# Optimization experiments

Measured on AMD Instinct MI355X. Metric: run time of the kernel, lower is better.

Reference implementation:

```python
import jax, jax.numpy as jnp
import numpy as np

B, OBS, LAT, NXT, E, HG, H = 8192, 128, 32, 128, 8, 256, 256


def setup_inputs() -> dict:
    key = jax.random.key(0)
    ks = jax.random.split(key, 20)
    d_in = OBS + LAT

    def w(k, shape, fan_in):
        return jax.random.uniform(k, shape, jnp.float32, -1.0, 1.0) * (np.sqrt(3.0) / np.sqrt(fan_in)).astype(np.float32)

    inp = {
        "x": jax.random.normal(ks[0], (B, OBS), jnp.float32),
        "z": jax.random.normal(ks[1], (B, LAT), jnp.float32),
        # gating MLP: (obs+lat) -> hg -> hg -> hg -> E
        "gw0": w(ks[2], (d_in, HG), d_in), "gb0": jnp.zeros((HG,), jnp.float32),
        "gw1": w(ks[3], (HG, HG), HG),    "gb1": jnp.zeros((HG,), jnp.float32),
        "gw2": w(ks[4], (HG, HG), HG),    "gb2": jnp.zeros((HG,), jnp.float32),
        "gw3": w(ks[5], (HG, E), HG),     "gb3": jnp.zeros((E,), jnp.float32),
        # expert weight stacks (kaiming-uniform-style init, bias = 0.01)
        "w0": w(ks[6], (E, d_in, H), d_in * H),      "b0": jnp.full((E, H), 0.01, jnp.float32),
        "w1": w(ks[7], (E, H + LAT, H), (H + LAT) * H), "b1": jnp.full((E, H), 0.01, jnp.float32),
        "w2": w(ks[8], (E, H + LAT, NXT), (H + LAT) * NXT), "b2": jnp.full((E, NXT), 0.01, jnp.float32),
    }
    return inp


def reference(x, z, gw0, gb0, gw1, gb1, gw2, gb2, gw3, gb3, w0, b0, w1, b1, w2, b2):
    xz = jnp.concatenate((x, z), axis=1)  # [B, obs+lat]
    # gating MLP (ELU activations, linear head) -> softmax coefficients over experts
    g = jax.nn.elu(xz @ gw0 + gb0)
    g = jax.nn.elu(g @ gw1 + gb1)
    g = jax.nn.elu(g @ gw2 + gb2)
    coef = jax.nn.softmax(g @ gw3 + gb3, axis=1)  # [B, E]

    layer_out = x
    for w, b, act in ((w0, b0, jax.nn.elu), (w1, b1, jax.nn.elu), (w2, b2, None)):
        inp = jnp.concatenate((layer_out, z), axis=1)  # [B, i]
        # coefficient-weighted expert mixing fused with the per-sample matvec:
        # equals (coef @ flat_weight).view(B,i,o) consumed by baddbmm in the original
        out = jnp.einsum('bi,eio,be->bo', inp, w, coef) + coef @ b
        layer_out = act(out) if act is not None else out
    return layer_out
```

## Files before the change

kernel.cpp:

```cpp
#include <hip/hip_runtime.h>
#include <hip/hip_bf16.h>

typedef _Float16 half_t;
typedef __attribute__((ext_vector_type(8))) _Float16 half8;
typedef __attribute__((ext_vector_type(4))) _Float16 half4;
typedef __attribute__((ext_vector_type(4))) float float4v;

#define BSZ 8192
#define NT 1024
#define ACTSTR 280
#define XSTR 152
#define ZSTR 40

#define RING_SLOT 1024
#define RING_WAVE (3 * RING_SLOT)
#define OFF_SX   (16 * RING_WAVE)
#define OFF_SB0  (OFF_SX + 32 * XSTR)
#define OFF_SB1  (OFF_SB0 + 32 * ACTSTR)
#define OFF_SZ   (OFF_SB1 + 32 * ACTSTR)
#define HALFS_TOTAL (OFF_SZ + 32 * ZSTR)
#define OFF_BIAS_B (HALFS_TOTAL * 2)
#define OFF_LOG_B  (OFF_BIAS_B + 8192)
#define OFF_CF_B   (OFF_LOG_B + 1024)
#define SMEM_BYTES (OFF_CF_B + 1024)

__device__ __forceinline__ float elu_fast(float v) {
    return v > 0.f ? v : (__expf(v) - 1.f);
}

template <int N>
__device__ __forceinline__ void wait_vm() {
    if constexpr (N == 0)      asm volatile("s_waitcnt vmcnt(0)" ::: "memory");
    else if constexpr (N == 1) asm volatile("s_waitcnt vmcnt(1)" ::: "memory");
    else if constexpr (N == 2) asm volatile("s_waitcnt vmcnt(2)" ::: "memory");
    else                       asm volatile("s_waitcnt vmcnt(4)" ::: "memory");
}

__device__ __forceinline__ void lds_dma16(half_t* lds, const half_t* g) {
    __builtin_amdgcn_global_load_lds(
        (const __attribute__((address_space(1))) void*)g,
        (__attribute__((address_space(3))) void*)lds, 16, 0, 0);
}

template <int EXPP, int NPASS, int CH, int MT, bool ZLAST, int ACT, int DST>
__device__ __forceinline__ void layer_run(
    half_t* sm, const half_t* sSrc, int sstr,
    const half_t* __restrict__ W, int NS,
    const float* __restrict__ bias, int biasN, const float* sCf, float* sBias,
    half_t* sDst, float* __restrict__ gOut, int ldg,
    int row0, int strip, int mrow, int wv, int lane, int l15, int quad) {
    constexpr int TOT = NPASS * CH;
    const size_t estr = (size_t)NS * CH * 512;
    const int col = strip * 16 + l15;
    half_t* ring = sm + wv * RING_WAVE;
    const half_t* sZ = sm + OFF_SZ;
    float* myBias = sBias + wv * 128;

    if (quad == 0) {
#pragma unroll
        for (int e = 0; e < NPASS * EXPP; ++e)
            myBias[e * 16 + l15] = bias[e * biasN + col];
    }
    wait_vm<0>();

    float4v acc[EXPP][MT];
    float part[MT][4];

    const half_t* wp = W + (size_t)strip * CH * 512 + lane * 8;
    int s_i = 0, c_i = 0;
    auto issue = [&]() {
        half_t* slot = ring + s_i * RING_SLOT;
#pragma unroll
        for (int e = 0; e < EXPP; ++e) lds_dma16(slot + e * 512, wp + (size_t)e * estr);
        s_i = (s_i == 2) ? 0 : s_i + 1;
        wp += 512;
        if (++c_i == CH) { c_i = 0; wp += EXPP * estr - CH * 512; }
    };

    const half_t* aBase = sSrc + (mrow + l15) * sstr + quad * 8;
    const half_t* zBase = sZ + (mrow + l15) * ZSTR + quad * 8;
    int s_c = 0, c_c = 0, h_c = 0;
    auto body = [&]() {
        half8 a[MT];
#pragma unroll
        for (int mt = 0; mt < MT; ++mt)
            a[mt] = (ZLAST && c_c == CH - 1)
                        ? *(const half8*)&zBase[mt * 16 * ZSTR]
                        : *(const half8*)&aBase[mt * 16 * sstr + c_c * 32];
        if (c_c == 0) {
#pragma unroll
            for (int e = 0; e < EXPP; ++e)
#pragma unroll
                for (int mt = 0; mt < MT; ++mt) acc[e][mt] = (float4v){0.f, 0.f, 0.f, 0.f};
        }
        const half_t* slot = ring + s_c * RING_SLOT + lane * 8;
#pragma unroll
        for (int e = 0; e < EXPP; ++e) {
            half8 b = *(const half8*)&slot[e * 512];
#pragma unroll
            for (int mt = 0; mt < MT; ++mt)
                acc[e][mt] = __builtin_amdgcn_mfma_f32_16x16x32_f16(a[mt], b, acc[e][mt], 0, 0, 0);
        }
        if (c_c == CH - 1) {
            const int eoff = h_c * EXPP;
#pragma unroll
            for (int mt = 0; mt < MT; ++mt)
#pragma unroll
                for (int r = 0; r < 4; ++r) {
                    const int rl = mrow + mt * 16 + quad * 4 + r;
                    float val = 0.f;
#pragma unroll
                    for (int e = 0; e < EXPP; ++e) {
                        const float ab = acc[e][mt][r] + myBias[(eoff + e) * 16 + l15];
                        val += (EXPP * NPASS == 1) ? ab : sCf[rl * 8 + eoff + e] * ab;
                    }
                    part[mt][r] = (h_c == 0) ? val : part[mt][r] + val;
                    if (h_c == NPASS - 1) {
                        float o = part[mt][r];
                        if (DST == 0) {
                            if (ACT) o = elu_fast(o);
                            sDst[rl * ACTSTR + col] = (half_t)o;
                        } else {
                            gOut[(size_t)(row0 + rl) * ldg + col] = o;
                        }
                    }
                }
        }
        s_c = (s_c == 2) ? 0 : s_c + 1;
        if (++c_c == CH) { c_c = 0; ++h_c; }
    };

    issue();
    issue();
#pragma unroll 1
    for (int it = 0; it < TOT - 2; ++it) {
        issue();
        wait_vm<2 * EXPP>();
        body();
    }
    wait_vm<EXPP>();
    body();
    wait_vm<0>();
    body();
}

__device__ __forceinline__ void layer_logits(
    const half_t* sSrc, const half_t* __restrict__ W,
    const float* __restrict__ bias, float* sLog, int wv, int lane, int l15, int quad) {
    if (wv != 0) return;
    float4v acc[2] = {(float4v){0.f, 0.f, 0.f, 0.f}, (float4v){0.f, 0.f, 0.f, 0.f}};
#pragma unroll
    for (int c = 0; c < 8; ++c) {
        half8 a0 = *(const half8*)&sSrc[l15 * ACTSTR + c * 32 + quad * 8];
        half8 a1 = *(const half8*)&sSrc[(16 + l15) * ACTSTR + c * 32 + quad * 8];
        half8 b = *(const half8*)&W[c * 512 + lane * 8];
        acc[0] = __builtin_amdgcn_mfma_f32_16x16x32_f16(a0, b, acc[0], 0, 0, 0);
        acc[1] = __builtin_amdgcn_mfma_f32_16x16x32_f16(a1, b, acc[1], 0, 0, 0);
    }
    if (l15 < 8) {
        const float bvv = bias[l15];
#pragma unroll
        for (int mt = 0; mt < 2; ++mt)
#pragma unroll
            for (int r = 0; r < 4; ++r)
                sLog[(mt * 16 + quad * 4 + r) * 8 + l15] = acc[mt][r] + bvv;
    }
}

__global__ __launch_bounds__(NT) void fused_mann(
    const float* __restrict__ x, const float* __restrict__ z,
    const half_t* __restrict__ Wg0, const half_t* __restrict__ Wg1,
    const half_t* __restrict__ Wg2, const half_t* __restrict__ Wg3,
    const float* __restrict__ gb0, const float* __restrict__ gb1,
    const float* __restrict__ gb2, const float* __restrict__ gb3,
    const half_t* __restrict__ W0, const half_t* __restrict__ W1,
    const half_t* __restrict__ W2, const float* __restrict__ b0,
    const float* __restrict__ b1, const float* __restrict__ b2,
    float* __restrict__ out) {
    extern __shared__ __align__(16) char dynsm[];
    half_t* sm = (half_t*)dynsm;
    half_t* sX = sm + OFF_SX;
    half_t* sB0 = sm + OFF_SB0;
    half_t* sB1 = sm + OFF_SB1;
    half_t* sZ = sm + OFF_SZ;
    float* sBias = (float*)(dynsm + OFF_BIAS_B);
    float* sLog = (float*)(dynsm + OFF_LOG_B);
    float* sCf = (float*)(dynsm + OFF_CF_B);

    const int tid = threadIdx.x;
    const int row0 = blockIdx.x * 32;
    const int lane = tid & 63, wv = tid >> 6;
    const int l15 = lane & 15, quad = lane >> 4;

    for (int i = tid; i < 32 * 128; i += NT) {
        int r = i >> 7, c = i & 127;
        sX[r * XSTR + c] = (half_t)x[(size_t)(row0 + r) * 128 + c];
    }
    for (int i = tid; i < 32 * 32; i += NT) {
        int r = i >> 5, c = i & 31;
        sZ[r * ZSTR + c] = (half_t)z[(size_t)(row0 + r) * 32 + c];
    }
    __syncthreads();

    layer_run<1, 1, 5, 2, true, 1, 0>(sm, sX, XSTR, Wg0, 16, gb0, 256, nullptr, sBias,
                                      sB0, nullptr, 0, row0, wv, 0, wv, lane, l15, quad);
    __syncthreads();
    layer_run<1, 1, 8, 2, false, 1, 0>(sm, sB0, ACTSTR, Wg1, 16, gb1, 256, nullptr, sBias,
                                       sB1, nullptr, 0, row0, wv, 0, wv, lane, l15, quad);
    __syncthreads();
    layer_run<1, 1, 8, 2, false, 1, 0>(sm, sB1, ACTSTR, Wg2, 16, gb2, 256, nullptr, sBias,
                                       sB0, nullptr, 0, row0, wv, 0, wv, lane, l15, quad);
    __syncthreads();
    layer_logits(sB0, Wg3, gb3, sLog, wv, lane, l15, quad);
    __syncthreads();
    if (tid < 32) {
        float v[8], m = -1e30f;
#pragma unroll
        for (int e = 0; e < 8; ++e) { v[e] = sLog[tid * 8 + e]; m = fmaxf(m, v[e]); }
        float sum = 0.f;
#pragma unroll
        for (int e = 0; e < 8; ++e) { v[e] = __expf(v[e] - m); sum += v[e]; }
        float inv = 1.f / sum;
#pragma unroll
        for (int e = 0; e < 8; ++e) sCf[tid * 8 + e] = v[e] * inv;
    }
    __syncthreads();
    layer_run<2, 4, 5, 2, true, 1, 0>(sm, sX, XSTR, W0, 16, b0, 256, sCf, sBias,
                                      sB1, nullptr, 0, row0, wv, 0, wv, lane, l15, quad);
    __syncthreads();
    layer_run<2, 4, 9, 2, true, 1, 0>(sm, sB1, ACTSTR, W1, 16, b1, 256, sCf, sBias,
                                      sB0, nullptr, 0, row0, wv, 0, wv, lane, l15, quad);
    __syncthreads();
    layer_run<2, 4, 9, 1, true, 0, 2>(sm, sB0, ACTSTR, W2, 8, b2, 128, sCf, sBias,
                                      nullptr, out, 128, row0, wv & 7, (wv >> 3) * 16,
                                      wv, lane, l15, quad);
}

struct WDesc { const float* src; half_t* dst; int K, N, Npad, blk0; };
struct WPack { WDesc d[7]; };

__global__ __launch_bounds__(256) void conv_w_all(WPack pk) {
    __shared__ float t[32][33];
    const int bid = blockIdx.x;
    int di = 0;
#pragma unroll
    for (int i = 1; i < 7; ++i)
        if (bid >= pk.d[i].blk0) di = i;
    const WDesc d = pk.d[di];
    const int NS = d.Npad >> 4, CHN = d.K >> 5;
    const int ntiles = d.Npad / 32, ktiles = CHN;
    int local = bid - d.blk0;
    const int e = local / (ktiles * ntiles);
    local %= ktiles * ntiles;
    const int k0 = (local / ntiles) * 32, n0 = (local % ntiles) * 32;
    const int tr = threadIdx.x >> 3;
    const int tc = (threadIdx.x & 7) * 4;

    float4 v = {0.f, 0.f, 0.f, 0.f};
    if (n0 + tc < d.N)
        v = *(const float4*)&d.src[((size_t)e * d.K + k0 + tr) * d.N + n0 + tc];
    t[tr][tc] = v.x; t[tr][tc + 1] = v.y; t[tr][tc + 2] = v.z; t[tr][tc + 3] = v.w;
    __syncthreads();
    half4 h;
#pragma unroll
    for (int i = 0; i < 4; ++i) h[i] = (half_t)t[tc + i][tr];
    const int n = n0 + tr;
    const size_t blk = ((size_t)e * NS + (n >> 4)) * CHN + (k0 >> 5);
    const int off = ((tc >> 3) * 16 + (n & 15)) * 8 + (tc & 7);
    *(half4*)&d.dst[blk * 512 + off] = h;
}

extern "C" void kernel_launch(void* const* d_in, const int* in_sizes, int n_in,
                              void* d_out, int out_size, void* d_ws, size_t ws_size,
                              hipStream_t stream) {
    const float* x   = (const float*)d_in[0];
    const float* z   = (const float*)d_in[1];
    const float* gw0 = (const float*)d_in[2];
    const float* gb0 = (const float*)d_in[3];
    const float* gw1 = (const float*)d_in[4];
    const float* gb1 = (const float*)d_in[5];
    const float* gw2 = (const float*)d_in[6];
    const float* gb2 = (const float*)d_in[7];
    const float* gw3 = (const float*)d_in[8];
    const float* gb3 = (const float*)d_in[9];
    const float* w0  = (const float*)d_in[10];
    const float* b0  = (const float*)d_in[11];
    const float* w1  = (const float*)d_in[12];
    const float* b1  = (const float*)d_in[13];
    const float* w2  = (const float*)d_in[14];
    const float* b2  = (const float*)d_in[15];

    char* p = (char*)d_ws;
    auto take = [&](size_t bytes) { char* r = p; p += bytes; return r; };
    half_t* Wg0 = (half_t*)take((size_t)256 * 160 * 2);
    half_t* Wg1 = (half_t*)take((size_t)256 * 256 * 2);
    half_t* Wg2 = (half_t*)take((size_t)256 * 256 * 2);
    half_t* Wg3 = (half_t*)take((size_t)32 * 256 * 2);
    half_t* W0  = (half_t*)take((size_t)8 * 256 * 160 * 2);
    half_t* W1  = (half_t*)take((size_t)8 * 256 * 288 * 2);
    half_t* W2  = (half_t*)take((size_t)8 * 128 * 288 * 2);
    float* out  = (float*)d_out;

    WPack pk;
    int blk = 0;
    auto mk = [&](int i, const float* s, half_t* dst, int K, int N, int Npad, int E) {
        pk.d[i] = WDesc{s, dst, K, N, Npad, blk};
        blk += E * (K / 32) * (Npad / 32);
    };
    mk(0, gw0, Wg0, 160, 256, 256, 1);
    mk(1, gw1, Wg1, 256, 256, 256, 1);
    mk(2, gw2, Wg2, 256, 256, 256, 1);
    mk(3, gw3, Wg3, 256, 8, 32, 1);
    mk(4, w0, W0, 160, 256, 256, 8);
    mk(5, w1, W1, 288, 256, 256, 8);
    mk(6, w2, W2, 288, 128, 128, 8);

    hipFuncSetAttribute((const void*)fused_mann,
                        hipFuncAttributeMaxDynamicSharedMemorySize, SMEM_BYTES);

    conv_w_all<<<dim3(blk), dim3(256), 0, stream>>>(pk);
    fused_mann<<<dim3(BSZ / 32), dim3(NT), SMEM_BYTES, stream>>>(
        x, z, Wg0, Wg1, Wg2, Wg3, gb0, gb1, gb2, gb3,
        W0, W1, W2, b0, b1, b2, out);
}
```

Measured before the change: 137.9 us.

## Replace LDS DMA weight ring with register double-buffered global loads

Weight tiles are now loaded directly from global memory into registers with a one-step prefetch, instead of being DMA'd into a per-wave three-slot LDS ring. Shared memory becomes static and shrinks substantially, removing the LDS round trip and possibly allowing more blocks per CU. In exchange, the prefetch distance is shorter and register pressure rises, which may expose memory latency.

```diff
diff --git a/kernel.cpp b/kernel.cpp
--- a/kernel.cpp
+++ b/kernel.cpp
@@ -12,39 +12,13 @@
 #define XSTR 152
 #define ZSTR 40
 
-#define RING_SLOT 1024
-#define RING_WAVE (3 * RING_SLOT)
-#define OFF_SX   (16 * RING_WAVE)
-#define OFF_SB0  (OFF_SX + 32 * XSTR)
-#define OFF_SB1  (OFF_SB0 + 32 * ACTSTR)
-#define OFF_SZ   (OFF_SB1 + 32 * ACTSTR)
-#define HALFS_TOTAL (OFF_SZ + 32 * ZSTR)
-#define OFF_BIAS_B (HALFS_TOTAL * 2)
-#define OFF_LOG_B  (OFF_BIAS_B + 8192)
-#define OFF_CF_B   (OFF_LOG_B + 1024)
-#define SMEM_BYTES (OFF_CF_B + 1024)
-
 __device__ __forceinline__ float elu_fast(float v) {
     return v > 0.f ? v : (__expf(v) - 1.f);
 }
 
-template <int N>
-__device__ __forceinline__ void wait_vm() {
-    if constexpr (N == 0)      asm volatile("s_waitcnt vmcnt(0)" ::: "memory");
-    else if constexpr (N == 1) asm volatile("s_waitcnt vmcnt(1)" ::: "memory");
-    else if constexpr (N == 2) asm volatile("s_waitcnt vmcnt(2)" ::: "memory");
-    else                       asm volatile("s_waitcnt vmcnt(4)" ::: "memory");
-}
-
-__device__ __forceinline__ void lds_dma16(half_t* lds, const half_t* g) {
-    __builtin_amdgcn_global_load_lds(
-        (const __attribute__((address_space(1))) void*)g,
-        (__attribute__((address_space(3))) void*)lds, 16, 0, 0);
-}
-
 template <int EXPP, int NPASS, int CH, int MT, bool ZLAST, int ACT, int DST>
 __device__ __forceinline__ void layer_run(
-    half_t* sm, const half_t* sSrc, int sstr,
+    const half_t* sSrc, int sstr, const half_t* sZ,
     const half_t* __restrict__ W, int NS,
     const float* __restrict__ bias, int biasN, const float* sCf, float* sBias,
     half_t* sDst, float* __restrict__ gOut, int ldg,
@@ -52,8 +26,6 @@
     constexpr int TOT = NPASS * CH;
     const size_t estr = (size_t)NS * CH * 512;
     const int col = strip * 16 + l15;
-    half_t* ring = sm + wv * RING_WAVE;
-    const half_t* sZ = sm + OFF_SZ;
     float* myBias = sBias + wv * 128;
 
     if (quad == 0) {
@@ -61,26 +33,29 @@
         for (int e = 0; e < NPASS * EXPP; ++e)
             myBias[e * 16 + l15] = bias[e * biasN + col];
     }
-    wait_vm<0>();
 
     float4v acc[EXPP][MT];
     float part[MT][4];
+    half8 bcur[EXPP], bnxt[EXPP];
 
     const half_t* wp = W + (size_t)strip * CH * 512 + lane * 8;
-    int s_i = 0, c_i = 0;
-    auto issue = [&]() {
-        half_t* slot = ring + s_i * RING_SLOT;
-#pragma unroll
-        for (int e = 0; e < EXPP; ++e) lds_dma16(slot + e * 512, wp + (size_t)e * estr);
-        s_i = (s_i == 2) ? 0 : s_i + 1;
-        wp += 512;
-        if (++c_i == CH) { c_i = 0; wp += EXPP * estr - CH * 512; }
-    };
+#pragma unroll
+    for (int e = 0; e < EXPP; ++e) bcur[e] = *(const half8*)&wp[(size_t)e * estr];
+    wp += 512;
+    int c_i = 1;
 
     const half_t* aBase = sSrc + (mrow + l15) * sstr + quad * 8;
     const half_t* zBase = sZ + (mrow + l15) * ZSTR + quad * 8;
-    int s_c = 0, c_c = 0, h_c = 0;
-    auto body = [&]() {
+    int c_c = 0, h_c = 0;
+
+#pragma unroll 1
+    for (int it = 0; it < TOT; ++it) {
+        if (it + 1 < TOT) {
+#pragma unroll
+            for (int e = 0; e < EXPP; ++e) bnxt[e] = *(const half8*)&wp[(size_t)e * estr];
+            wp += 512;
+            if (++c_i == CH) { c_i = 0; wp += EXPP * estr - (size_t)CH * 512; }
+        }
         half8 a[MT];
 #pragma unroll
         for (int mt = 0; mt < MT; ++mt)
@@ -93,14 +68,12 @@
 #pragma unroll
                 for (int mt = 0; mt < MT; ++mt) acc[e][mt] = (float4v){0.f, 0.f, 0.f, 0.f};
         }
-        const half_t* slot = ring + s_c * RING_SLOT + lane * 8;
-#pragma unroll
-        for (int e = 0; e < EXPP; ++e) {
-            half8 b = *(const half8*)&slot[e * 512];
+#pragma unroll
+        for (int e = 0; e < EXPP; ++e)
 #pragma unroll
             for (int mt = 0; mt < MT; ++mt)
-                acc[e][mt] = __builtin_amdgcn_mfma_f32_16x16x32_f16(a[mt], b, acc[e][mt], 0, 0, 0);
-        }
+                acc[e][mt] = __builtin_amdgcn_mfma_f32_16x16x32_f16(a[mt], bcur[e],
+                                                                    acc[e][mt], 0, 0, 0);
         if (c_c == CH - 1) {
             const int eoff = h_c * EXPP;
 #pragma unroll
@@ -126,22 +99,10 @@
                     }
                 }
         }
-        s_c = (s_c == 2) ? 0 : s_c + 1;
         if (++c_c == CH) { c_c = 0; ++h_c; }
-    };
-
-    issue();
-    issue();
-#pragma unroll 1
-    for (int it = 0; it < TOT - 2; ++it) {
-        issue();
-        wait_vm<2 * EXPP>();
-        body();
-    }
-    wait_vm<EXPP>();
-    body();
-    wait_vm<0>();
-    body();
+#pragma unroll
+        for (int e = 0; e < EXPP; ++e) bcur[e] = bnxt[e];
+    }
 }
 
 __device__ __forceinline__ void layer_logits(
@@ -177,15 +138,13 @@
     const half_t* __restrict__ W2, const float* __restrict__ b0,
     const float* __restrict__ b1, const float* __restrict__ b2,
     float* __restrict__ out) {
-    extern __shared__ __align__(16) char dynsm[];
-    half_t* sm = (half_t*)dynsm;
-    half_t* sX = sm + OFF_SX;
-    half_t* sB0 = sm + OFF_SB0;
-    half_t* sB1 = sm + OFF_SB1;
-    half_t* sZ = sm + OFF_SZ;
-    float* sBias = (float*)(dynsm + OFF_BIAS_B);
-    float* sLog = (float*)(dynsm + OFF_LOG_B);
-    float* sCf = (float*)(dynsm + OFF_CF_B);
+    __shared__ __align__(16) half_t sX[32 * XSTR];
+    __shared__ __align__(16) half_t sB0[32 * ACTSTR];
+    __shared__ __align__(16) half_t sB1[32 * ACTSTR];
+    __shared__ __align__(16) half_t sZ[32 * ZSTR];
+    __shared__ float sBias[16 * 128];
+    __shared__ float sLog[256];
+    __shared__ float sCf[256];
 
     const int tid = threadIdx.x;
     const int row0 = blockIdx.x * 32;
@@ -202,13 +161,13 @@
     }
     __syncthreads();
 
-    layer_run<1, 1, 5, 2, true, 1, 0>(sm, sX, XSTR, Wg0, 16, gb0, 256, nullptr, sBias,
+    layer_run<1, 1, 5, 2, true, 1, 0>(sX, XSTR, sZ, Wg0, 16, gb0, 256, nullptr, sBias,
                                       sB0, nullptr, 0, row0, wv, 0, wv, lane, l15, quad);
     __syncthreads();
-    layer_run<1, 1, 8, 2, false, 1, 0>(sm, sB0, ACTSTR, Wg1, 16, gb1, 256, nullptr, sBias,
+    layer_run<1, 1, 8, 2, false, 1, 0>(sB0, ACTSTR, sZ, Wg1, 16, gb1, 256, nullptr, sBias,
                                        sB1, nullptr, 0, row0, wv, 0, wv, lane, l15, quad);
     __syncthreads();
-    layer_run<1, 1, 8, 2, false, 1, 0>(sm, sB1, ACTSTR, Wg2, 16, gb2, 256, nullptr, sBias,
+    layer_run<1, 1, 8, 2, false, 1, 0>(sB1, ACTSTR, sZ, Wg2, 16, gb2, 256, nullptr, sBias,
                                        sB0, nullptr, 0, row0, wv, 0, wv, lane, l15, quad);
     __syncthreads();
     layer_logits(sB0, Wg3, gb3, sLog, wv, lane, l15, quad);
@@ -225,13 +184,13 @@
         for (int e = 0; e < 8; ++e) sCf[tid * 8 + e] = v[e] * inv;
     }
     __syncthreads();
-    layer_run<2, 4, 5, 2, true, 1, 0>(sm, sX, XSTR, W0, 16, b0, 256, sCf, sBias,
+    layer_run<2, 4, 5, 2, true, 1, 0>(sX, XSTR, sZ, W0, 16, b0, 256, sCf, sBias,
                                       sB1, nullptr, 0, row0, wv, 0, wv, lane, l15, quad);
     __syncthreads();
-    layer_run<2, 4, 9, 2, true, 1, 0>(sm, sB1, ACTSTR, W1, 16, b1, 256, sCf, sBias,
+    layer_run<2, 4, 9, 2, true, 1, 0>(sB1, ACTSTR, sZ, W1, 16, b1, 256, sCf, sBias,
                                       sB0, nullptr, 0, row0, wv, 0, wv, lane, l15, quad);
     __syncthreads();
-    layer_run<2, 4, 9, 1, true, 0, 2>(sm, sB0, ACTSTR, W2, 8, b2, 128, sCf, sBias,
+    layer_run<2, 4, 9, 1, true, 0, 2>(sB0, ACTSTR, sZ, W2, 8, b2, 128, sCf, sBias,
                                       nullptr, out, 128, row0, wv & 7, (wv >> 3) * 16,
                                       wv, lane, l15, quad);
 }
@@ -315,11 +274,8 @@
     mk(5, w1, W1, 288, 256, 256, 8);
     mk(6, w2, W2, 288, 128, 128, 8);
 
-    hipFuncSetAttribute((const void*)fused_mann,
-                        hipFuncAttributeMaxDynamicSharedMemorySize, SMEM_BYTES);
-
     conv_w_all<<<dim3(blk), dim3(256), 0, stream>>>(pk);
-    fused_mann<<<dim3(BSZ / 32), dim3(NT), SMEM_BYTES, stream>>>(
+    fused_mann<<<dim3(BSZ / 32), dim3(NT), 0, stream>>>(
         x, z, Wg0, Wg1, Wg2, Wg3, gb0, gb1, gb2, gb3,
         W0, W1, W2, b0, b1, b2, out);
 }
```

After: 145.8 us. 1.06x slower.
